# Performance work log

Measured on AMD Instinct MI355X. Metric: run time of the kernel, lower is better.

## Reference

```python
import jax, jax.numpy as jnp
import numpy as np

N, E, IN, H, OUT = 50000, 600000, 256, 128, 40
EPS, GAMMA = 0.1, 0.1  # PyG AntiSymmetricConv defaults


def _build_norm(edge_index, n):
    # GCNConv normalization with added self loops: D^-1/2 (A+I) D^-1/2
    loops = jnp.arange(n, dtype=edge_index.dtype)
    src = jnp.concatenate([edge_index[0], loops])
    dst = jnp.concatenate([edge_index[1], loops])
    deg = jax.ops.segment_sum(jnp.ones(src.shape[0], dtype=jnp.float32), dst, num_segments=n)
    dinv = jnp.where(deg > 0, jax.lax.rsqrt(jnp.maximum(deg, 1e-12)), 0.0)
    return src, dst, dinv[src] * dinv[dst]


def _gcn(x, w, src, dst, norm, n):
    # GCNConv(bias=False): scatter normalized messages to target nodes
    m = (x @ w)[src] * norm[:, None]          # [E+N, d]
    return jax.ops.segment_sum(m, dst, num_segments=n)


def _antisym_conv(x, W, gcn_w, bias, src, dst, norm, num_iters):
    d = W.shape[0]
    aW = W - W.T - GAMMA * jnp.eye(d, dtype=W.dtype)  # antisymmetric weight
    n = x.shape[0]

    def step(h, _):
        upd = jnp.tanh(h @ aW.T + _gcn(h, gcn_w, src, dst, norm, n) + bias)
        return h + EPS * upd, None

    x, _ = jax.lax.scan(step, x, None, length=num_iters)
    return x


def setup_inputs() -> dict:
    key = jax.random.key(0)
    ks = jax.random.split(key, 16)
    s = lambda fan: 1.0 / np.sqrt(fan)
    return {
        "x": jax.random.normal(ks[0], (N, IN), dtype=jnp.float32),
        "edge_index": jax.random.randint(ks[1], (2, E), 0, N, dtype=jnp.int64),
        "w_hid": jax.random.normal(ks[2], (H, IN), dtype=jnp.float32) * s(IN),
        "b_hid": jax.random.normal(ks[3], (H,), dtype=jnp.float32) * s(IN),
        "W_a1": jax.random.normal(ks[4], (H, H), dtype=jnp.float32) * s(H),
        "gcn_w1": jax.random.normal(ks[5], (H, H), dtype=jnp.float32) * s(H),
        "b_a1": jax.random.normal(ks[6], (H,), dtype=jnp.float32) * s(H),
        "w_hid2": jax.random.normal(ks[7], (H // 2, H), dtype=jnp.float32) * s(H),
        "b_hid2": jax.random.normal(ks[8], (H // 2,), dtype=jnp.float32) * s(H),
        "W_a2": jax.random.normal(ks[9], (H // 2, H // 2), dtype=jnp.float32) * s(H // 2),
        "gcn_w2": jax.random.normal(ks[10], (H // 2, H // 2), dtype=jnp.float32) * s(H // 2),
        "b_a2": jax.random.normal(ks[11], (H // 2,), dtype=jnp.float32) * s(H // 2),
        "w_fc": jax.random.normal(ks[12], (OUT, H // 2), dtype=jnp.float32) * s(H // 2),
        "b_fc": jax.random.normal(ks[13], (OUT,), dtype=jnp.float32) * s(H // 2),
    }


def reference(x, edge_index, w_hid, b_hid, W_a1, gcn_w1, b_a1,
              w_hid2, b_hid2, W_a2, gcn_w2, b_a2, w_fc, b_fc):
    n = x.shape[0]
    src, dst, norm = _build_norm(edge_index, n)
    h = jax.nn.leaky_relu(x @ w_hid.T + b_hid)          # dropout is no-op in eval
    h = _antisym_conv(h, W_a1, gcn_w1, b_a1, src, dst, norm, num_iters=3)
    h = jax.nn.leaky_relu(h)
    h = jax.nn.leaky_relu(h @ w_hid2.T + b_hid2)
    h = _antisym_conv(h, W_a2, gcn_w2, b_a2, src, dst, norm, num_iters=1)
    out = h @ w_fc.T + b_fc
    return jax.nn.log_softmax(out, axis=1)
```

## Files before the change

### kernel.cpp

```cpp
#include <hip/hip_runtime.h>
#include <hip/hip_bf16.h>
#include <math.h>

typedef unsigned short u16;
typedef unsigned int   u32;
using short8  = __attribute__((ext_vector_type(8))) short;
using f32x4   = __attribute__((ext_vector_type(4))) float;
using f32x2   = __attribute__((ext_vector_type(2))) float;

static constexpr int NNODE = 50000;
static constexpr int NEDGE = 600000;
static constexpr float EPSC   = 0.1f;
static constexpr float GAMMAC = 0.1f;

static constexpr int NTILE = (NNODE + 63) / 64;
static constexpr int GH    = 128;
static constexpr int NRNG  = 12500;
static constexpr int NWORD = NRNG / 2;
static constexpr int NPASS = 4;

static constexpr long long O_DINV   = 0;
static constexpr long long O_DEGI   = 50000;
static constexpr long long O_ROWPTR = 100000;
static constexpr long long O_GCUR   = 150004;
static constexpr long long O_ECSR   = 200260;
static constexpr long long O_WHB    = 1400260;
static constexpr long long O_G1TB   = O_WHB  + 16384;
static constexpr long long O_AW1B   = O_G1TB + 8192;
static constexpr long long O_W2B    = O_AW1B + 8192;
static constexpr long long O_AW2B   = O_W2B  + 4096;
static constexpr long long O_G2TB   = O_AW2B + 2048;
static constexpr long long O_WFCB   = O_G2TB + 2048;
static constexpr long long O_AGGB   = 3450004;
static constexpr long long O_HB0    = O_AGGB + 3200000;
static constexpr long long O_HB1    = O_HB0  + 3200000;
static constexpr long long O_S0     = O_HB1  + 3200000;
static constexpr long long O_S1     = O_S0   + 1600000;
static constexpr long long O_PART   = O_S1   + 1600000;
static constexpr long long O_BASE   = O_PART + 3200000;

__device__ __forceinline__ float bf2f(u16 u) {
    return __uint_as_float(((unsigned)u) << 16);
}
__device__ __forceinline__ u16 f2bf(float f) {
    unsigned u = __float_as_uint(f);
    return (u16)((u + 0x7FFFu + ((u >> 16) & 1u)) >> 16);
}
__device__ __forceinline__ float ftanh(float x) {
    float x2 = fminf(fmaxf(2.f * x, -30.f), 30.f);
    float e = __expf(x2);
    return (e - 1.f) * __builtin_amdgcn_rcpf(e + 1.f);
}
__device__ __forceinline__ u16 pk_fp8(float a, float b) {
    int pk = __builtin_amdgcn_cvt_pk_fp8_f32(a, b, 0, false);
    return (u16)(pk & 0xffff);
}
__device__ __forceinline__ void acc_fp8x4(float* a, u32 v, float w) {
    f32x2 lo = __builtin_amdgcn_cvt_pk_f32_fp8(v, false);
    f32x2 hi = __builtin_amdgcn_cvt_pk_f32_fp8(v, true);
    a[0] += lo[0] * w;
    a[1] += lo[1] * w;
    a[2] += hi[0] * w;
    a[3] += hi[1] * w;
}

__global__ __launch_bounds__(256) void prep_kernel(
    const float* __restrict__ w_hid, const float* __restrict__ W_a1,
    const float* __restrict__ gcn1,  const float* __restrict__ w2,
    const float* __restrict__ W_a2,  const float* __restrict__ gcn2,
    const float* __restrict__ wfc,   float* __restrict__ ws)
{
    int j = blockIdx.x * 256 + threadIdx.x;
    if (j < 32768) { ((u16*)(ws+O_WHB))[j] = f2bf(w_hid[j]); return; } j -= 32768;
    if (j < 16384) { int r=j>>7, c=j&127; ((u16*)(ws+O_G1TB))[j] = f2bf(gcn1[c*128+r]); return; } j -= 16384;
    if (j < 16384) { int r=j>>7, c=j&127;
                     ((u16*)(ws+O_AW1B))[j] = f2bf(W_a1[r*128+c] - W_a1[c*128+r] - (r==c?GAMMAC:0.f));
                     return; } j -= 16384;
    if (j < 8192)  { ((u16*)(ws+O_W2B))[j] = f2bf(w2[j]); return; } j -= 8192;
    if (j < 4096)  { int r=j>>6, c=j&63;
                     ((u16*)(ws+O_AW2B))[j] = f2bf(W_a2[r*64+c] - W_a2[c*64+r] - (r==c?GAMMAC:0.f));
                     return; } j -= 4096;
    if (j < 4096)  { int r=j>>6, c=j&63; ((u16*)(ws+O_G2TB))[j] = f2bf(gcn2[c*64+r]); return; } j -= 4096;
    if (j < 2560)  { ((u16*)(ws+O_WFCB))[j] = f2bf(wfc[j]); return; } j -= 2560;
    if (j == 0)    { ((int*)(ws+O_GCUR))[0] = 0; }
}

__global__ __launch_bounds__(256) void alloc_kernel(
    const u16* __restrict__ part, float* __restrict__ dinv,
    int* __restrict__ degi, int* __restrict__ rowptr,
    u16* __restrict__ base16, int* __restrict__ gcur)
{
    int i = blockIdx.x * 256 + threadIdx.x;
    int lane = threadIdx.x & 63;
    bool ok = i < NNODE;
    int deg = 0;
    if (ok) {
        int run = 0;
        #pragma unroll 4
        for (int g = 0; g < GH; ++g) {
            base16[(long long)g * NNODE + i] = (u16)run;
            run += part[(long long)g * NNODE + i];
        }
        deg = run;
        degi[i] = deg;
        dinv[i] = rsqrtf(1.0f + (float)deg);
    }
    int run = deg;
    #pragma unroll
    for (int off = 1; off < 64; off <<= 1) {
        int v = __shfl_up(run, off);
        if (lane >= off) run += v;
    }
    int tot = __shfl(run, 63);
    int basep = 0;
    if (lane == 63) basep = atomicAdd(gcur, tot);
    basep = __shfl(basep, 63);
    if (ok) rowptr[i] = basep + run - deg;
}

__global__ __launch_bounds__(256) void fill_kernel(
    const int* __restrict__ ei, const float* __restrict__ dinv,
    const int* __restrict__ rowptr, const u16* __restrict__ base16,
    int2* __restrict__ ecsr)
{
    __shared__ u32 cur[NWORD];
    const int g    = blockIdx.x >> 2;
    const int pass = blockIdx.x & 3;
    const long long e0 = (long long)g * NEDGE / GH;
    const long long e1 = (long long)(g + 1) * NEDGE / GH;
    const u16* bb = base16 + (long long)g * NNODE;
    const int nbase = pass * NRNG;
    for (int wi = threadIdx.x; wi < NWORD; wi += 256) cur[wi] = 0;
    __syncthreads();
    for (long long e = e0 + threadIdx.x; e < e1; e += 256) {
        int d = ei[NEDGE + e];
        int r = d - nbase;
        if ((unsigned)r < (unsigned)NRNG) {
            int s = ei[e];
            u32 old = atomicAdd(&cur[r >> 1], 1u << ((r & 1) * 16));
            int rank = (int)((old >> ((r & 1) * 16)) & 0xffffu);
            int slot = rowptr[d] + (int)bb[d] + rank;
            int2 v;
            v.x = s;
            v.y = __float_as_int(dinv[s]);
            ecsr[slot] = v;
        }
    }
}

template<int KS, int NT, int AF32, int LOADACT, int EPI>
__global__ __launch_bounds__(256, 4) void mgemm(
    const void* __restrict__ Araw,
    const u16* __restrict__ Bt,
    const float* __restrict__ bias,
    float* __restrict__ outF,
    u16* __restrict__ outB,
    u16* __restrict__ outB8,
    int M, int Nn, int ldc,
    const int* __restrict__ ei,
    u16* __restrict__ partial)
{
    constexpr int K    = KS * 32;
    constexpr int KCHU = (K > 128) ? 128 : K;
    constexpr int KC   = KCHU / 32;
    constexpr int NCH  = K / KCHU;
    constexpr int P    = KCHU + 8;
    constexpr int ROWS = NT * 16;
    constexpr int CW   = NT * 16 + 1;
    constexpr int BSZ  = ROWS * P * 2;
    constexpr int ASZ  = 64 * CW * 4;
    constexpr int SMEM = BSZ > ASZ ? BSZ : ASZ;
    __shared__ __align__(16) char smem[SMEM];

    if (ei && blockIdx.x >= NTILE) {
        int g = blockIdx.x - NTILE;
        u32* hist = (u32*)smem;
        const long long e0 = (long long)g * NEDGE / GH;
        const long long e1 = (long long)(g + 1) * NEDGE / GH;
        u16* part = partial + (long long)g * NNODE;
        for (int pass = 0; pass < NPASS; ++pass) {
            const int nbase = pass * NRNG;
            for (int wi = threadIdx.x; wi < NWORD; wi += 256) hist[wi] = 0;
            __syncthreads();
            for (long long e = e0 + threadIdx.x; e < e1; e += 256) {
                int d = ei[NEDGE + e];
                int r = d - nbase;
                if ((unsigned)r < (unsigned)NRNG)
                    atomicAdd(&hist[r >> 1], 1u << ((r & 1) * 16));
            }
            __syncthreads();
            for (int wi = threadIdx.x; wi < NWORD; wi += 256)
                *(u32*)&part[nbase + wi * 2] = hist[wi];
            __syncthreads();
        }
        return;
    }

    u16*   bl   = (u16*)smem;
    float* accL = (float*)smem;

    const int wave = threadIdx.x >> 6;
    const int lane = threadIdx.x & 63;
    const int m = lane & 15, q = lane >> 4;
    const int rowbase = blockIdx.x * 64 + wave * 16;
    const int row = rowbase + m;
    const bool rok = row < M;
    const short8 z8 = {0,0,0,0,0,0,0,0};

    short8 af[KS];
    if (AF32) {
        const float* apf = (const float*)Araw + (long long)row * K;
        #pragma unroll
        for (int k = 0; k < KS; ++k) {
            short8 t = z8;
            if (rok) {
                const float4* p = (const float4*)(apf + (k * 4 + q) * 8);
                float4 a = p[0], b = p[1];
                t[0]=(short)f2bf(a.x); t[1]=(short)f2bf(a.y); t[2]=(short)f2bf(a.z); t[3]=(short)f2bf(a.w);
                t[4]=(short)f2bf(b.x); t[5]=(short)f2bf(b.y); t[6]=(short)f2bf(b.z); t[7]=(short)f2bf(b.w);
            }
            af[k] = t;
        }
    } else {
        const short8* ap = (const short8*)((const u16*)Araw + (long long)row * K);
        #pragma unroll
        for (int k = 0; k < KS; ++k) af[k] = rok ? ap[k * 4 + q] : z8;
    }
    if (LOADACT) {
        #pragma unroll
        for (int k = 0; k < KS; ++k)
            #pragma unroll
            for (int e = 0; e < 8; ++e) {
                float f = bf2f((u16)af[k][e]);
                f = f > 0.f ? f : 0.01f * f;
                af[k][e] = (short)f2bf(f);
            }
    }

    f32x4 acc[NT];
    #pragma unroll
    for (int j = 0; j < NT; ++j) acc[j] = (f32x4){0.f,0.f,0.f,0.f};

    for (int ch = 0; ch < NCH; ++ch) {
        if (ch) __syncthreads();
        constexpr int CHUNKS = ROWS * (KCHU / 8);
        for (int t = threadIdx.x; t < CHUNKS; t += 256) {
            int r = t / (KCHU / 8), c = t - r * (KCHU / 8);
            short8 v = z8;
            if (r < Nn) v = *(const short8*)&Bt[(long long)r * K + ch * KCHU + c * 8];
            *(short8*)&bl[r * P + c * 8] = v;
        }
        __syncthreads();
        #pragma unroll
        for (int j = 0; j < NT; ++j) {
            #pragma unroll
            for (int k = 0; k < KC; ++k) {
                short8 bf_ = *(const short8*)&bl[(j * 16 + m) * P + k * 32 + q * 8];
                acc[j] = __builtin_amdgcn_mfma_f32_16x16x32_bf16(af[ch * KC + k], bf_, acc[j], 0, 0, 0);
            }
        }
    }

    __syncthreads();
    #pragma unroll
    for (int j = 0; j < NT; ++j)
        #pragma unroll
        for (int r = 0; r < 4; ++r)
            accL[(wave * 16 + q * 4 + r) * CW + j * 16 + m] = acc[j][r];
    __syncthreads();

    const int c0 = lane * 2;
    if (c0 < NT * 16) {
        float2 bv = {0.f, 0.f};
        if (bias) {
            if (c0 < Nn)     bv.x = bias[c0];
            if (c0 + 1 < Nn) bv.y = bias[c0 + 1];
        }
        #pragma unroll
        for (int rl = 0; rl < 16; ++rl) {
            int rowD = rowbase + rl;
            if (rowD >= M) continue;
            float2 v = *(const float2*)&accL[(wave * 16 + rl) * CW + c0];
            long long o = (long long)rowD * ldc + c0;
            v.x += bv.x; v.y += bv.y;
            if (EPI == 1) {
                v.x = v.x > 0.f ? v.x : 0.01f * v.x;
                v.y = v.y > 0.f ? v.y : 0.01f * v.y;
            }
            if (c0 + 1 < Nn) {
                if (outB) { ushort2 ob; ob.x = f2bf(v.x); ob.y = f2bf(v.y);
                            *(ushort2*)&outB[o] = ob; }
                if (outB8) outB8[o >> 1] = pk_fp8(v.x, v.y);
                if (outF) { *(float2*)&outF[o] = v; }
            } else if (c0 < Nn) {
                if (outB) outB[o] = f2bf(v.x);
                if (outF) outF[o] = v.x;
            }
        }
    }
}

template<int HD>
__global__ __launch_bounds__(256) void gather_kernel(
    const int* __restrict__ rowptr, const int* __restrict__ degi,
    const int2* __restrict__ ecsr, const float* __restrict__ dinv,
    const u32* __restrict__ g8, u16* __restrict__ aggB)
{
    int node = (blockIdx.x * 256 + threadIdx.x) >> 6;
    int lane = threadIdx.x & 63;
    if (node >= NNODE) return;
    const int qr = lane >> 4, l4 = lane & 15;
    const int r0 = rowptr[node];
    const int r1 = r0 + degi[node];
    const float dn = dinv[node];
    constexpr int EL = (HD == 128) ? 8 : 4;

    float a[EL];
    #pragma unroll
    for (int i = 0; i < EL; ++i) a[i] = 0.f;
    if (qr == 0) {
        if (HD == 128) {
            uint2 gv = ((const uint2*)g8)[(long long)node * 16 + l4];
            acc_fp8x4(a, gv.x, dn);
            acc_fp8x4(a + 4, gv.y, dn);
        } else {
            u32 gv = g8[(long long)node * 16 + l4];
            acc_fp8x4(a, gv, dn);
        }
    }

    for (int base = r0; base < r1; base += 64) {
        int idx = base + lane;
        int cs = 0; float cw = 0.f;
        if (idx < r1) { int2 ev = ecsr[idx]; cs = ev.x; cw = __int_as_float(ev.y); }
        int cnt = min(64, r1 - base);
        for (int j = 0; j < cnt; j += 16) {
            #pragma unroll
            for (int u = 0; u < 4; ++u) {
                int jj = j + u * 4 + qr;
                int   s = __shfl(cs, jj);
                float w = __shfl(cw, jj);
                if (HD == 128) {
                    uint2 gv = ((const uint2*)g8)[(long long)s * 16 + l4];
                    acc_fp8x4(a, gv.x, w);
                    acc_fp8x4(a + 4, gv.y, w);
                } else {
                    u32 gv = g8[(long long)s * 16 + l4];
                    acc_fp8x4(a, gv, w);
                }
            }
        }
    }

    #pragma unroll
    for (int i = 0; i < EL; ++i) {
        a[i] += __shfl_xor(a[i], 16);
        a[i] += __shfl_xor(a[i], 32);
    }
    if (HD == 128) {
        float v0 = (qr == 0) ? a[0] : (qr == 1) ? a[2] : (qr == 2) ? a[4] : a[6];
        float v1 = (qr == 0) ? a[1] : (qr == 1) ? a[3] : (qr == 2) ? a[5] : a[7];
        v0 *= dn; v1 *= dn;
        long long o = (long long)node * 128 + l4 * 8 + qr * 2;
        ushort2 ob; ob.x = f2bf(v0); ob.y = f2bf(v1);
        *(ushort2*)&aggB[o] = ob;
    } else {
        float v = (qr == 0) ? a[0] : (qr == 1) ? a[1] : (qr == 2) ? a[2] : a[3];
        aggB[(long long)node * 64 + l4 * 4 + qr] = f2bf(v * dn);
    }
}

template<int TAIL>
__global__ __launch_bounds__(512, 3) void fconv(
    const u16* __restrict__ hA, const u32* __restrict__ g8,
    const int* __restrict__ rowptr, const int* __restrict__ degi,
    const int2* __restrict__ ecsr, const float* __restrict__ dinv,
    const u16* __restrict__ BtW, const u16* __restrict__ BtG,
    const float* __restrict__ bias,
    u16* __restrict__ outB, u16* __restrict__ outB8,
    const u16* __restrict__ w2W, const float* __restrict__ b2)
{
    constexpr int K = 128, P = 136;
    __shared__ __align__(16) char smem[52224];
    u16* bl   = (u16*)smem;
    u16* aggT = (u16*)(smem + 34816);
    const int wave = threadIdx.x >> 6, lane = threadIdx.x & 63;
    const int m = lane & 15, q = lane >> 4;
    const int blockrow = blockIdx.x * 64;
    const short8 z8 = {0,0,0,0,0,0,0,0};

    {
        const int qr = q, l4 = m;
        for (int nn = 0; nn < 8; ++nn) {
            int lr = wave * 8 + nn;
            int node = blockrow + lr;
            if (node >= NNODE) break;
            const int r0 = rowptr[node];
            const int r1 = r0 + degi[node];
            const float dn = dinv[node];
            float a[8] = {0.f,0.f,0.f,0.f,0.f,0.f,0.f,0.f};
            if (qr == 0) {
                uint2 gv = ((const uint2*)g8)[(long long)node * 16 + l4];
                acc_fp8x4(a, gv.x, dn);
                acc_fp8x4(a + 4, gv.y, dn);
            }
            for (int base = r0; base < r1; base += 64) {
                int idx = base + lane;
                int cs = 0; float cw = 0.f;
                if (idx < r1) { int2 ev = ecsr[idx]; cs = ev.x; cw = __int_as_float(ev.y); }
                int cnt = min(64, r1 - base);
                for (int j = 0; j < cnt; j += 16) {
                    #pragma unroll
                    for (int u = 0; u < 4; ++u) {
                        int jj = j + u * 4 + qr;
                        int   s = __shfl(cs, jj);
                        float w = __shfl(cw, jj);
                        uint2 gv = ((const uint2*)g8)[(long long)s * 16 + l4];
                        acc_fp8x4(a, gv.x, w);
                        acc_fp8x4(a + 4, gv.y, w);
                    }
                }
            }
            #pragma unroll
            for (int i = 0; i < 8; ++i) {
                a[i] += __shfl_xor(a[i], 16);
                a[i] += __shfl_xor(a[i], 32);
            }
            float v0 = (qr == 0) ? a[0] : (qr == 1) ? a[2] : (qr == 2) ? a[4] : a[6];
            float v1 = (qr == 0) ? a[1] : (qr == 1) ? a[3] : (qr == 2) ? a[5] : a[7];
            v0 *= dn; v1 *= dn;
            ushort2 ob; ob.x = f2bf(v0); ob.y = f2bf(v1);
            *(ushort2*)&aggT[lr * P + l4 * 8 + qr * 2] = ob;
        }
    }
    __syncthreads();

    const int nh = wave >> 2;
    const int rowbase = blockrow + (wave & 3) * 16;
    const int row = rowbase + m;
    const bool rok = row < NNODE;

    short8 af1[4], af2[4];
    {
        const short8* ap1 = (const short8*)(hA + (long long)row * K);
        #pragma unroll
        for (int k = 0; k < 4; ++k) {
            af1[k] = rok ? ap1[k * 4 + q] : z8;
            af2[k] = rok ? *(const short8*)&aggT[((wave & 3) * 16 + m) * P + k * 32 + q * 8] : z8;
        }
    }

    f32x4 acc[4];
    #pragma unroll
    for (int j = 0; j < 4; ++j) acc[j] = (f32x4){0.f,0.f,0.f,0.f};

    #pragma unroll
    for (int pass = 0; pass < 2; ++pass) {
        const u16* Bsrc = pass ? BtG : BtW;
        if (pass) __syncthreads();
        for (int t = threadIdx.x; t < 2048; t += 512) {
            int r = t >> 4, c = t & 15;
            *(short8*)&bl[r * P + c * 8] = *(const short8*)&Bsrc[(long long)r * K + c * 8];
        }
        __syncthreads();
        #pragma unroll
        for (int j = 0; j < 4; ++j)
            #pragma unroll
            for (int kk = 0; kk < 4; ++kk) {
                short8 b_ = *(const short8*)&bl[(nh*64 + j*16 + m) * P + kk*32 + q*8];
                acc[j] = __builtin_amdgcn_mfma_f32_16x16x32_bf16(
                    pass ? af2[kk] : af1[kk], b_, acc[j], 0, 0, 0);
            }
    }

    __syncthreads();
    float* accW = (float*)smem + wave * 16 * 65;
    #pragma unroll
    for (int j = 0; j < 4; ++j)
        #pragma unroll
        for (int r = 0; r < 4; ++r)
            accW[(q*4 + r) * 65 + j*16 + m] = acc[j][r];

    const int hw = lane >> 5;
    const int c0 = (lane & 31) * 2;
    float2 bv = {bias[nh*64 + c0], bias[nh*64 + c0 + 1]};

    if (TAIL == 0) {
        #pragma unroll
        for (int rl8 = 0; rl8 < 8; ++rl8) {
            int rl = hw * 8 + rl8;
            int rowD = rowbase + rl;
            if (rowD >= NNODE) continue;
            float2 v = *(const float2*)&accW[rl * 65 + c0];
            long long o = (long long)rowD * 128 + nh*64 + c0;
            ushort2 hh = *(const ushort2*)&hA[o];
            float n0 = bf2f(hh.x) + EPSC * ftanh(v.x + bv.x);
            float n1 = bf2f(hh.y) + EPSC * ftanh(v.y + bv.y);
            ushort2 ob; ob.x = f2bf(n0); ob.y = f2bf(n1);
            *(ushort2*)&outB[o] = ob;
            outB8[o >> 1] = pk_fp8(n0, n1);
        }
        return;
    }

    #pragma unroll
    for (int rl8 = 0; rl8 < 8; ++rl8) {
        int rl = hw * 8 + rl8;
        int rowD = rowbase + rl;
        float n0 = 0.f, n1 = 0.f;
        if (rowD < NNODE) {
            float2 v = *(const float2*)&accW[rl * 65 + c0];
            long long o = (long long)rowD * 128 + nh*64 + c0;
            ushort2 hh = *(const ushort2*)&hA[o];
            n0 = bf2f(hh.x) + EPSC * ftanh(v.x + bv.x);
            n1 = bf2f(hh.y) + EPSC * ftanh(v.y + bv.y);
            n0 = n0 > 0.f ? n0 : 0.01f * n0;
            n1 = n1 > 0.f ? n1 : 0.01f * n1;
        }
        ushort2 ob; ob.x = f2bf(n0); ob.y = f2bf(n1);
        *(ushort2*)&aggT[((wave & 3) * 16 + rl) * P + nh*64 + c0] = ob;
    }
    __syncthreads();

    short8 af3[4];
    #pragma unroll
    for (int k = 0; k < 4; ++k)
        af3[k] = *(const short8*)&aggT[((wave & 3) * 16 + m) * P + k * 32 + q * 8];

    for (int t = threadIdx.x; t < 1024; t += 512) {
        int r = t >> 4, c = t & 15;
        *(short8*)&bl[r * P + c * 8] = *(const short8*)&w2W[(long long)r * K + c * 8];
    }
    __syncthreads();

    f32x4 acc2[2];
    #pragma unroll
    for (int j = 0; j < 2; ++j) acc2[j] = (f32x4){0.f,0.f,0.f,0.f};
    #pragma unroll
    for (int j = 0; j < 2; ++j)
        #pragma unroll
        for (int k = 0; k < 4; ++k) {
            short8 b_ = *(const short8*)&bl[(nh*32 + j*16 + m) * P + k*32 + q*8];
            acc2[j] = __builtin_amdgcn_mfma_f32_16x16x32_bf16(af3[k], b_, acc2[j], 0, 0, 0);
        }

    __syncthreads();
    float* accW2 = (float*)smem + wave * 16 * 33;
    #pragma unroll
    for (int j = 0; j < 2; ++j)
        #pragma unroll
        for (int r = 0; r < 4; ++r)
            accW2[(q*4 + r) * 33 + j*16 + m] = acc2[j][r];

    const int r4 = lane >> 4;
    const int c2 = (lane & 15) * 2;
    float2 bv2 = {b2[nh*32 + c2], b2[nh*32 + c2 + 1]};
    #pragma unroll
    for (int rr = 0; rr < 4; ++rr) {
        int rl = r4 * 4 + rr;
        int rowD = rowbase + rl;
        if (rowD >= NNODE) continue;
        float2 v = *(const float2*)&accW2[rl * 33 + c2];
        v.x += bv2.x; v.y += bv2.y;
        v.x = v.x > 0.f ? v.x : 0.01f * v.x;
        v.y = v.y > 0.f ? v.y : 0.01f * v.y;
        long long o = (long long)rowD * 64 + nh*32 + c2;
        ushort2 ob; ob.x = f2bf(v.x); ob.y = f2bf(v.y);
        *(ushort2*)&outB[o] = ob;
        outB8[o >> 1] = pk_fp8(v.x, v.y);
    }
}

__global__ __launch_bounds__(256, 4) void conv2fc(
    const u16* __restrict__ hA,
    const u16* __restrict__ gA,
    const u16* __restrict__ BtW, const u16* __restrict__ BtG,
    const float* __restrict__ bias,
    const u16* __restrict__ wfcB, const float* __restrict__ bfc,
    float* __restrict__ outF, int M)
{
    constexpr int K  = 64, NT = 4, KS = 2;
    constexpr int P  = K + 8;
    constexpr int CW = 65;
    constexpr int R1 = 64 * CW * 4;
    __shared__ __align__(16) char smem[R1 + 64 * P * 2];
    u16*   bl   = (u16*)smem;
    float* accL = (float*)smem;
    u16*   aggT = (u16*)(smem + R1);

    const int wave = threadIdx.x >> 6;
    const int lane = threadIdx.x & 63;
    const int m = lane & 15, q = lane >> 4;
    const int rowbase = blockIdx.x * 64 + wave * 16;
    const int row = rowbase + m;
    const bool rok = row < M;
    const short8 z8 = {0,0,0,0,0,0,0,0};

    short8 af1[KS], af2[KS];
    {
        const short8* ap1 = (const short8*)(hA + (long long)row * K);
        const short8* ap2 = (const short8*)(gA + (long long)row * K);
        #pragma unroll
        for (int k = 0; k < KS; ++k) {
            af1[k] = rok ? ap1[k * 4 + q] : z8;
            af2[k] = rok ? ap2[k * 4 + q] : z8;
        }
    }

    f32x4 acc[NT];
    #pragma unroll
    for (int j = 0; j < NT; ++j) acc[j] = (f32x4){0.f,0.f,0.f,0.f};

    #pragma unroll
    for (int pass = 0; pass < 2; ++pass) {
        const u16* Bcur = pass ? BtG : BtW;
        if (pass) __syncthreads();
        constexpr int CHUNKS = 64 * (K / 8);
        for (int t = threadIdx.x; t < CHUNKS; t += 256) {
            int r = t >> 3, c = t & 7;
            *(short8*)&bl[r * P + c * 8] = *(const short8*)&Bcur[(long long)r * K + c * 8];
        }
        __syncthreads();
        #pragma unroll
        for (int j = 0; j < NT; ++j)
            #pragma unroll
            for (int k = 0; k < KS; ++k) {
                short8 bf_ = *(const short8*)&bl[(j * 16 + m) * P + k * 32 + q * 8];
                acc[j] = __builtin_amdgcn_mfma_f32_16x16x32_bf16(
                    pass ? af2[k] : af1[k], bf_, acc[j], 0, 0, 0);
            }
    }

    __syncthreads();
    #pragma unroll
    for (int j = 0; j < NT; ++j)
        #pragma unroll
        for (int r = 0; r < 4; ++r)
            accL[(wave * 16 + q * 4 + r) * CW + j * 16 + m] = acc[j][r];
    __syncthreads();

    {
        const int c0 = lane * 2;
        float2 bv = {bias[c0 & 63], bias[(c0 + 1) & 63]};
        if (c0 < 64) {
            #pragma unroll
            for (int rl = 0; rl < 16; ++rl) {
                int rowD = rowbase + rl;
                float n0 = 0.f, n1 = 0.f;
                if (rowD < M) {
                    float2 v = *(const float2*)&accL[(wave * 16 + rl) * CW + c0];
                    long long o = (long long)rowD * 64 + c0;
                    ushort2 hh = *(const ushort2*)&hA[o];
                    n0 = bf2f(hh.x) + EPSC * ftanh(v.x + bv.x);
                    n1 = bf2f(hh.y) + EPSC * ftanh(v.y + bv.y);
                }
                ushort2 ob; ob.x = f2bf(n0); ob.y = f2bf(n1);
                *(ushort2*)&aggT[(wave * 16 + rl) * P + c0] = ob;
            }
        }
    }
    __syncthreads();

    short8 af4[KS];
    #pragma unroll
    for (int k = 0; k < KS; ++k)
        af4[k] = *(const short8*)&aggT[(wave * 16 + m) * P + k * 32 + q * 8];

    {
        constexpr int CHF = 48 * 8;
        for (int t = threadIdx.x; t < CHF; t += 256) {
            int r = t >> 3, c = t & 7;
            short8 v = z8;
            if (r < 40) v = *(const short8*)&wfcB[(long long)r * K + c * 8];
            *(short8*)&bl[r * P + c * 8] = v;
        }
    }
    __syncthreads();

    f32x4 acc3[3];
    #pragma unroll
    for (int j = 0; j < 3; ++j) acc3[j] = (f32x4){0.f,0.f,0.f,0.f};
    #pragma unroll
    for (int j = 0; j < 3; ++j)
        #pragma unroll
        for (int k = 0; k < KS; ++k) {
            short8 bf_ = *(const short8*)&bl[(j * 16 + m) * P + k * 32 + q * 8];
            acc3[j] = __builtin_amdgcn_mfma_f32_16x16x32_bf16(af4[k], bf_, acc3[j], 0, 0, 0);
        }

    __syncthreads();
    constexpr int CW3 = 49;
    #pragma unroll
    for (int j = 0; j < 3; ++j)
        #pragma unroll
        for (int r = 0; r < 4; ++r)
            accL[(wave * 16 + q * 4 + r) * CW3 + j * 16 + m] = acc3[j][r];
    __syncthreads();

    float mrow = 0.f, lrow = 0.f;
    if (lane < 16) {
        const float* rp = &accL[(wave * 16 + lane) * CW3];
        float mx = -1e30f;
        for (int c = 0; c < 40; ++c) mx = fmaxf(mx, rp[c] + bfc[c]);
        float s = 0.f;
        for (int c = 0; c < 40; ++c) s += expf(rp[c] + bfc[c] - mx);
        mrow = mx; lrow = logf(s);
    }
    for (int rl = 0; rl < 16; ++rl) {
        float mm = __shfl(mrow, rl);
        float ll = __shfl(lrow, rl);
        int rowD = rowbase + rl;
        if (rowD < M && lane < 40) {
            float v = accL[(wave * 16 + rl) * CW3 + lane] + bfc[lane];
            outF[(long long)rowD * 40 + lane] = v - mm - ll;
        }
    }
}

extern "C" void kernel_launch(void* const* d_in, const int* in_sizes, int n_in,
                              void* d_out, int out_size, void* d_ws, size_t ws_size,
                              hipStream_t stream) {
    const float* x     = (const float*)d_in[0];
    const int*   ei    = (const int*)d_in[1];
    const float* w_hid = (const float*)d_in[2];
    const float* b_hid = (const float*)d_in[3];
    const float* W_a1  = (const float*)d_in[4];
    const float* gcn1  = (const float*)d_in[5];
    const float* b_a1  = (const float*)d_in[6];
    const float* w2    = (const float*)d_in[7];
    const float* b2    = (const float*)d_in[8];
    const float* W_a2  = (const float*)d_in[9];
    const float* gcn2  = (const float*)d_in[10];
    const float* b_a2  = (const float*)d_in[11];
    const float* wfc   = (const float*)d_in[12];
    const float* bfc   = (const float*)d_in[13];
    float* ws = (float*)d_ws;
    float* out = (float*)d_out;

    float* dinv   = ws + O_DINV;
    int*   degi   = (int*)(ws + O_DEGI);
    int*   rowptr = (int*)(ws + O_ROWPTR);
    int*   gcur   = (int*)(ws + O_GCUR);
    int2*  ecsr   = (int2*)(ws + O_ECSR);
    u16* whB  = (u16*)(ws + O_WHB);
    u16* g1tB = (u16*)(ws + O_G1TB);
    u16* aw1B = (u16*)(ws + O_AW1B);
    u16* w2B  = (u16*)(ws + O_W2B);
    u16* aw2B = (u16*)(ws + O_AW2B);
    u16* g2tB = (u16*)(ws + O_G2TB);
    u16* wfcB = (u16*)(ws + O_WFCB);
    u16* aggB = (u16*)(ws + O_AGGB);
    u16* hB0  = (u16*)(ws + O_HB0);
    u16* hB1  = (u16*)(ws + O_HB1);
    u16* s0   = (u16*)(ws + O_S0);
    u16* s1   = (u16*)(ws + O_S1);
    u16* part = (u16*)(ws + O_PART);
    u16* base16 = (u16*)(ws + O_BASE);

    prep_kernel<<<(84481 + 255) / 256, 256, 0, stream>>>(
        w_hid, W_a1, gcn1, w2, W_a2, gcn2, wfc, ws);

    const int gatherBlocks = (NNODE * 64 + 255) / 256;

    mgemm<8, 8, 1, 0, 1><<<NTILE + GH, 256, 0, stream>>>(
        x, whB, b_hid, nullptr, hB0, s0, NNODE, 128, 128, ei, part);

    alloc_kernel<<<(NNODE + 255) / 256, 256, 0, stream>>>(
        part, dinv, degi, rowptr, base16, gcur);
    fill_kernel<<<GH * NPASS, 256, 0, stream>>>(ei, dinv, rowptr, base16, ecsr);

    fconv<0><<<NTILE, 512, 0, stream>>>(hB0, (const u32*)s0, rowptr, degi, ecsr, dinv,
                                        aw1B, g1tB, b_a1, hB1, s1, nullptr, nullptr);
    fconv<0><<<NTILE, 512, 0, stream>>>(hB1, (const u32*)s1, rowptr, degi, ecsr, dinv,
                                        aw1B, g1tB, b_a1, hB0, s0, nullptr, nullptr);
    fconv<1><<<NTILE, 512, 0, stream>>>(hB0, (const u32*)s0, rowptr, degi, ecsr, dinv,
                                        aw1B, g1tB, b_a1, hB1, s1, w2B, b2);

    gather_kernel<64><<<gatherBlocks, 256, 0, stream>>>(
        rowptr, degi, ecsr, dinv, (const u32*)s1, aggB);
    conv2fc<<<NTILE, 256, 0, stream>>>(
        hB1, aggB, aw2B, g2tB, b_a2, wfcB, bfc, out, NNODE);
}
```

Before: 358.1 us.

## Fuse second-layer neighbor gather into conv2fc kernel via shared-memory aggregate

Removes the standalone gather kernel for the 64-wide second conv and folds the edge aggregation into a new fused kernel (fconv2). Each 512-thread block first gathers aggregated fp8 neighbor features for its 64 nodes into shared memory, then runs the antisymmetric and GCN MFMAs, the tanh update and the FC plus log-softmax. This avoids one kernel launch and the global write and read of the aggregate buffer, and splits output columns across wave halves. The cost is that the gather now runs inside a block with fewer parallel nodes per wave, which may hurt latency hiding.

Measured after the change: 365.0 us. About the same (+1.9%).

```diff
diff --git a/kernel.cpp b/kernel.cpp
--- a/kernel.cpp
+++ b/kernel.cpp
@@ -300,76 +300,6 @@
     }
 }
 
-template<int HD>
-__global__ __launch_bounds__(256) void gather_kernel(
-    const int* __restrict__ rowptr, const int* __restrict__ degi,
-    const int2* __restrict__ ecsr, const float* __restrict__ dinv,
-    const u32* __restrict__ g8, u16* __restrict__ aggB)
-{
-    int node = (blockIdx.x * 256 + threadIdx.x) >> 6;
-    int lane = threadIdx.x & 63;
-    if (node >= NNODE) return;
-    const int qr = lane >> 4, l4 = lane & 15;
-    const int r0 = rowptr[node];
-    const int r1 = r0 + degi[node];
-    const float dn = dinv[node];
-    constexpr int EL = (HD == 128) ? 8 : 4;
-
-    float a[EL];
-    #pragma unroll
-    for (int i = 0; i < EL; ++i) a[i] = 0.f;
-    if (qr == 0) {
-        if (HD == 128) {
-            uint2 gv = ((const uint2*)g8)[(long long)node * 16 + l4];
-            acc_fp8x4(a, gv.x, dn);
-            acc_fp8x4(a + 4, gv.y, dn);
-        } else {
-            u32 gv = g8[(long long)node * 16 + l4];
-            acc_fp8x4(a, gv, dn);
-        }
-    }
-
-    for (int base = r0; base < r1; base += 64) {
-        int idx = base + lane;
-        int cs = 0; float cw = 0.f;
-        if (idx < r1) { int2 ev = ecsr[idx]; cs = ev.x; cw = __int_as_float(ev.y); }
-        int cnt = min(64, r1 - base);
-        for (int j = 0; j < cnt; j += 16) {
-            #pragma unroll
-            for (int u = 0; u < 4; ++u) {
-                int jj = j + u * 4 + qr;
-                int   s = __shfl(cs, jj);
-                float w = __shfl(cw, jj);
-                if (HD == 128) {
-                    uint2 gv = ((const uint2*)g8)[(long long)s * 16 + l4];
-                    acc_fp8x4(a, gv.x, w);
-                    acc_fp8x4(a + 4, gv.y, w);
-                } else {
-                    u32 gv = g8[(long long)s * 16 + l4];
-                    acc_fp8x4(a, gv, w);
-                }
-            }
-        }
-    }
-
-    #pragma unroll
-    for (int i = 0; i < EL; ++i) {
-        a[i] += __shfl_xor(a[i], 16);
-        a[i] += __shfl_xor(a[i], 32);
-    }
-    if (HD == 128) {
-        float v0 = (qr == 0) ? a[0] : (qr == 1) ? a[2] : (qr == 2) ? a[4] : a[6];
-        float v1 = (qr == 0) ? a[1] : (qr == 1) ? a[3] : (qr == 2) ? a[5] : a[7];
-        v0 *= dn; v1 *= dn;
-        long long o = (long long)node * 128 + l4 * 8 + qr * 2;
-        ushort2 ob; ob.x = f2bf(v0); ob.y = f2bf(v1);
-        *(ushort2*)&aggB[o] = ob;
-    } else {
-        float v = (qr == 0) ? a[0] : (qr == 1) ? a[1] : (qr == 2) ? a[2] : a[3];
-        aggB[(long long)node * 64 + l4 * 4 + qr] = f2bf(v * dn);
-    }
-}
-
 template<int TAIL>
 __global__ __launch_bounds__(512, 3) void fconv(
     const u16* __restrict__ hA, const u32* __restrict__ g8,
@@ -571,147 +501,182 @@
     }
 }
 
-__global__ __launch_bounds__(256, 4) void conv2fc(
+__global__ __launch_bounds__(512, 3) void fconv2(
     const u16* __restrict__ hA,
-    const u16* __restrict__ gA,
+    const u32* __restrict__ g8,
+    const int* __restrict__ rowptr, const int* __restrict__ degi,
+    const int2* __restrict__ ecsr, const float* __restrict__ dinv,
     const u16* __restrict__ BtW, const u16* __restrict__ BtG,
     const float* __restrict__ bias,
     const u16* __restrict__ wfcB, const float* __restrict__ bfc,
-    float* __restrict__ outF, int M)
+    float* __restrict__ outF)
 {
-    constexpr int K  = 64, NT = 4, KS = 2;
-    constexpr int P  = K + 8;
-    constexpr int CW = 65;
-    constexpr int R1 = 64 * CW * 4;
-    __shared__ __align__(16) char smem[R1 + 64 * P * 2];
-    u16*   bl   = (u16*)smem;
-    float* accL = (float*)smem;
-    u16*   aggT = (u16*)(smem + R1);
-
-    const int wave = threadIdx.x >> 6;
-    const int lane = threadIdx.x & 63;
+    constexpr int P = 72;
+    __shared__ __align__(16) char smem[44288];
+    u16*   bl    = (u16*)smem;
+    u16*   aggT  = (u16*)(smem + 18432);
+    float* accL  = (float*)(smem + 27648);
+    float* accL3 = (float*)(smem + 27648);
+    const int wave = threadIdx.x >> 6, lane = threadIdx.x & 63;
     const int m = lane & 15, q = lane >> 4;
-    const int rowbase = blockIdx.x * 64 + wave * 16;
+    const int blockrow = blockIdx.x * 64;
+    const short8 z8 = {0,0,0,0,0,0,0,0};
+
+    {
+        const int qr = q, l4 = m;
+        for (int nn = 0; nn < 8; ++nn) {
+            int lr = wave * 8 + nn;
+            int node = blockrow + lr;
+            if (node >= NNODE) { aggT[lr * P + l4 * 4 + qr] = 0; continue; }
+            const int r0 = rowptr[node];
+            const int r1 = r0 + degi[node];
+            const float dn = dinv[node];
+            float a[4] = {0.f,0.f,0.f,0.f};
+            if (qr == 0) {
+                u32 gv = g8[(long long)node * 16 + l4];
+                acc_fp8x4(a, gv, dn);
+            }
+            for (int base = r0; base < r1; base += 64) {
+                int idx = base + lane;
+                int cs = 0; float cw = 0.f;
+                if (idx < r1) { int2 ev = ecsr[idx]; cs = ev.x; cw = __int_as_float(ev.y); }
+                int cnt = min(64, r1 - base);
+                for (int j = 0; j < cnt; j += 16) {
+                    #pragma unroll
+                    for (int u = 0; u < 4; ++u) {
+                        int jj = j + u * 4 + qr;
+                        int   s = __shfl(cs, jj);
+                        float w = __shfl(cw, jj);
+                        u32 gv = g8[(long long)s * 16 + l4];
+                        acc_fp8x4(a, gv, w);
+                    }
+                }
+            }
+            #pragma unroll
+            for (int i = 0; i < 4; ++i) {
+                a[i] += __shfl_xor(a[i], 16);
+                a[i] += __shfl_xor(a[i], 32);
+            }
+            float v = (qr == 0) ? a[0] : (qr == 1) ? a[1] : (qr == 2) ? a[2] : a[3];
+            aggT[lr * P + l4 * 4 + qr] = f2bf(v * dn);
+        }
+    }
+    __syncthreads();
+
+    const int rq = wave & 3, nh = wave >> 2;
+    const int rowbase = blockrow + rq * 16;
     const int row = rowbase + m;
-    const bool rok = row < M;
-    const short8 z8 = {0,0,0,0,0,0,0,0};
-
-    short8 af1[KS], af2[KS];
+    const bool rok = row < NNODE;
+
+    short8 af1[2], af2[2];
     {
-        const short8* ap1 = (const short8*)(hA + (long long)row * K);
-        const short8* ap2 = (const short8*)(gA + (long long)row * K);
-        #pragma unroll
-        for (int k = 0; k < KS; ++k) {
+        const short8* ap1 = (const short8*)(hA + (long long)row * 64);
+        #pragma unroll
+        for (int k = 0; k < 2; ++k) {
             af1[k] = rok ? ap1[k * 4 + q] : z8;
-            af2[k] = rok ? ap2[k * 4 + q] : z8;
-        }
-    }
-
-    f32x4 acc[NT];
-    #pragma unroll
-    for (int j = 0; j < NT; ++j) acc[j] = (f32x4){0.f,0.f,0.f,0.f};
-
-    #pragma unroll
-    for (int pass = 0; pass < 2; ++pass) {
-        const u16* Bcur = pass ? BtG : BtW;
-        if (pass) __syncthreads();
-        constexpr int CHUNKS = 64 * (K / 8);
-        for (int t = threadIdx.x; t < CHUNKS; t += 256) {
-            int r = t >> 3, c = t & 7;
-            *(short8*)&bl[r * P + c * 8] = *(const short8*)&Bcur[(long long)r * K + c * 8];
-        }
-        __syncthreads();
-        #pragma unroll
-        for (int j = 0; j < NT; ++j)
+            af2[k] = *(const short8*)&aggT[(rq * 16 + m) * P + k * 32 + q * 8];
+        }
+    }
+
+    for (int t = threadIdx.x; t < 1024; t += 512) {
+        int r = t >> 3, c = t & 7;
+        const u16* src = (r < 64) ? &BtW[(long long)r * 64 + c * 8]
+                                  : &BtG[(long long)(r - 64) * 64 + c * 8];
+        *(short8*)&bl[r * P + c * 8] = *(const short8*)src;
+    }
+    __syncthreads();
+
+    f32x4 acc[2];
+    acc[0] = (f32x4){0.f,0.f,0.f,0.f};
+    acc[1] = (f32x4){0.f,0.f,0.f,0.f};
+    #pragma unroll
+    for (int pass = 0; pass < 2; ++pass)
+        #pragma unroll
+        for (int j = 0; j < 2; ++j)
             #pragma unroll
-            for (int k = 0; k < KS; ++k) {
-                short8 bf_ = *(const short8*)&bl[(j * 16 + m) * P + k * 32 + q * 8];
+            for (int k = 0; k < 2; ++k) {
+                short8 b_ = *(const short8*)&bl[(pass*64 + nh*32 + j*16 + m) * P + k*32 + q*8];
                 acc[j] = __builtin_amdgcn_mfma_f32_16x16x32_bf16(
-                    pass ? af2[k] : af1[k], bf_, acc[j], 0, 0, 0);
-            }
-    }
-
-    __syncthreads();
-    #pragma unroll
-    for (int j = 0; j < NT; ++j)
+                    pass ? af2[k] : af1[k], b_, acc[j], 0, 0, 0);
+            }
+
+    #pragma unroll
+    for (int j = 0; j < 2; ++j)
         #pragma unroll
         for (int r = 0; r < 4; ++r)
-            accL[(wave * 16 + q * 4 + r) * CW + j * 16 + m] = acc[j][r];
+            accL[(rq*16 + q*4 + r) * 65 + nh*32 + j*16 + m] = acc[j][r];
     __syncthreads();
 
     {
-        const int c0 = lane * 2;
-        float2 bv = {bias[c0 & 63], bias[(c0 + 1) & 63]};
-        if (c0 < 64) {
+        const int hw = lane >> 5;
+        const int c0 = (lane & 31) * 2;
+        float2 bv = {bias[c0], bias[c0 + 1]};
+        #pragma unroll
+        for (int rr = 0; rr < 4; ++rr) {
+            int rl = wave * 8 + hw * 4 + rr;
+            int rowD = blockrow + rl;
+            float n0 = 0.f, n1 = 0.f;
+            if (rowD < NNODE) {
+                float2 v = *(const float2*)&accL[rl * 65 + c0];
+                long long o = (long long)rowD * 64 + c0;
+                ushort2 hh = *(const ushort2*)&hA[o];
+                n0 = bf2f(hh.x) + EPSC * ftanh(v.x + bv.x);
+                n1 = bf2f(hh.y) + EPSC * ftanh(v.y + bv.y);
+            }
+            ushort2 ob; ob.x = f2bf(n0); ob.y = f2bf(n1);
+            *(ushort2*)&aggT[rl * P + c0] = ob;
+        }
+    }
+    __syncthreads();
+
+    short8 af4[2];
+    #pragma unroll
+    for (int k = 0; k < 2; ++k)
+        af4[k] = *(const short8*)&aggT[(rq * 16 + m) * P + k * 32 + q * 8];
+
+    for (int t = threadIdx.x; t < 384; t += 512) {
+        int r = t >> 3, c = t & 7;
+        short8 v = z8;
+        if (r < 40) v = *(const short8*)&wfcB[(long long)r * 64 + c * 8];
+        *(short8*)&bl[r * P + c * 8] = v;
+    }
+    __syncthreads();
+
+    f32x4 acc3[3];
+    #pragma unroll
+    for (int j = 0; j < 3; ++j) acc3[j] = (f32x4){0.f,0.f,0.f,0.f};
+    #pragma unroll
+    for (int j = 0; j < 3; ++j)
+        #pragma unroll
+        for (int k = 0; k < 2; ++k) {
+            short8 b_ = *(const short8*)&bl[(j*16 + m) * P + k*32 + q*8];
+            acc3[j] = __builtin_amdgcn_mfma_f32_16x16x32_bf16(af4[k], b_, acc3[j], 0, 0, 0);
+        }
+
+    if (nh == 0) {
+        #pragma unroll
+        for (int j = 0; j < 3; ++j)
             #pragma unroll
-            for (int rl = 0; rl < 16; ++rl) {
-                int rowD = rowbase + rl;
-                float n0 = 0.f, n1 = 0.f;
-                if (rowD < M) {
-                    float2 v = *(const float2*)&accL[(wave * 16 + rl) * CW + c0];
-                    long long o = (long long)rowD * 64 + c0;
-                    ushort2 hh = *(const ushort2*)&hA[o];
-                    n0 = bf2f(hh.x) + EPSC * ftanh(v.x + bv.x);
-                    n1 = bf2f(hh.y) + EPSC * ftanh(v.y + bv.y);
-                }
-                ushort2 ob; ob.x = f2bf(n0); ob.y = f2bf(n1);
-                *(ushort2*)&aggT[(wave * 16 + rl) * P + c0] = ob;
-            }
-        }
-    }
-    __syncthreads();
-
-    short8 af4[KS];
-    #pragma unroll
-    for (int k = 0; k < KS; ++k)
-        af4[k] = *(const short8*)&aggT[(wave * 16 + m) * P + k * 32 + q * 8];
-
-    {
-        constexpr int CHF = 48 * 8;
-        for (int t = threadIdx.x; t < CHF; t += 256) {
-            int r = t >> 3, c = t & 7;
-            short8 v = z8;
-            if (r < 40) v = *(const short8*)&wfcB[(long long)r * K + c * 8];
-            *(short8*)&bl[r * P + c * 8] = v;
-        }
-    }
-    __syncthreads();
-
-    f32x4 acc3[3];
-    #pragma unroll
-    for (int j = 0; j < 3; ++j) acc3[j] = (f32x4){0.f,0.f,0.f,0.f};
-    #pragma unroll
-    for (int j = 0; j < 3; ++j)
-        #pragma unroll
-        for (int k = 0; k < KS; ++k) {
-            short8 bf_ = *(const short8*)&bl[(j * 16 + m) * P + k * 32 + q * 8];
-            acc3[j] = __builtin_amdgcn_mfma_f32_16x16x32_bf16(af4[k], bf_, acc3[j], 0, 0, 0);
-        }
-
-    __syncthreads();
-    constexpr int CW3 = 49;
-    #pragma unroll
-    for (int j = 0; j < 3; ++j)
-        #pragma unroll
-        for (int r = 0; r < 4; ++r)
-            accL[(wave * 16 + q * 4 + r) * CW3 + j * 16 + m] = acc3[j][r];
+            for (int r = 0; r < 4; ++r)
+                accL3[(rq*16 + q*4 + r) * 49 + j*16 + m] = acc3[j][r];
+    }
     __syncthreads();
 
     float mrow = 0.f, lrow = 0.f;
-    if (lane < 16) {
-        const float* rp = &accL[(wave * 16 + lane) * CW3];
+    if (lane < 8) {
+        const float* rp = &accL3[(wave * 8 + lane) * 49];
         float mx = -1e30f;
         for (int c = 0; c < 40; ++c) mx = fmaxf(mx, rp[c] + bfc[c]);
         float s = 0.f;
         for (int c = 0; c < 40; ++c) s += expf(rp[c] + bfc[c] - mx);
         mrow = mx; lrow = logf(s);
     }
-    for (int rl = 0; rl < 16; ++rl) {
+    for (int rl = 0; rl < 8; ++rl) {
         float mm = __shfl(mrow, rl);
         float ll = __shfl(lrow, rl);
-        int rowD = rowbase + rl;
-        if (rowD < M && lane < 40) {
-            float v = accL[(wave * 16 + rl) * CW3 + lane] + bfc[lane];
+        int rowD = blockrow + wave * 8 + rl;
+        if (rowD < NNODE && lane < 40) {
+            float v = accL3[(wave * 8 + rl) * 49 + lane] + bfc[lane];
             outF[(long long)rowD * 40 + lane] = v - mm - ll;
         }
     }
@@ -749,7 +714,6 @@
     u16* aw2B = (u16*)(ws + O_AW2B);
     u16* g2tB = (u16*)(ws + O_G2TB);
     u16* wfcB = (u16*)(ws + O_WFCB);
-    u16* aggB = (u16*)(ws + O_AGGB);
     u16* hB0  = (u16*)(ws + O_HB0);
     u16* hB1  = (u16*)(ws + O_HB1);
     u16* s0   = (u16*)(ws + O_S0);
@@ -760,8 +724,6 @@
     prep_kernel<<<(84481 + 255) / 256, 256, 0, stream>>>(
         w_hid, W_a1, gcn1, w2, W_a2, gcn2, wfc, ws);
 
-    const int gatherBlocks = (NNODE * 64 + 255) / 256;
-
     mgemm<8, 8, 1, 0, 1><<<NTILE + GH, 256, 0, stream>>>(
         x, whB, b_hid, nullptr, hB0, s0, NNODE, 128, 128, ei, part);
 
@@ -776,8 +738,6 @@
     fconv<1><<<NTILE, 512, 0, stream>>>(hB0, (const u32*)s0, rowptr, degi, ecsr, dinv,
                                         aw1B, g1tB, b_a1, hB1, s1, w2B, b2);
 
-    gather_kernel<64><<<gatherBlocks, 256, 0, stream>>>(
-        rowptr, degi, ecsr, dinv, (const u32*)s1, aggB);
-    conv2fc<<<NTILE, 256, 0, stream>>>(
-        hB1, aggB, aw2B, g2tB, b_a2, wfcB, bfc, out, NNODE);
-}
+    fconv2<<<NTILE, 512, 0, stream>>>(hB1, (const u32*)s1, rowptr, degi, ecsr, dinv,
+                                      aw2B, g2tB, b_a2, wfcB, bfc, out);
+}
```
